# Kernel optimization log

Hardware: AMD Instinct MI355X
Metric: run time of the kernel (lower is better)

Reference implementation:

```python
import jax, jax.numpy as jnp
import numpy as np

N = 50000
EPS = 1e-4
NUM_CLASSES = 10
PROTOS_PER_CLASS = 5


def setup_inputs() -> dict:
    key = jax.random.key(0)
    ks = jax.random.split(key, 12)
    x = jax.random.normal(ks[0], (N, 512), dtype=jnp.float32)
    edge_index = jax.random.randint(ks[1], (2, 640000), 0, N, dtype=jnp.int64)
    # GCNConv weights (PyG: y = x @ W^T + b after aggregation)
    def glorot(k, o, i):
        s = jnp.sqrt(6.0 / (o + i)).astype(jnp.float32)
        return jax.random.uniform(k, (o, i), jnp.float32, -s, s)
    W1 = glorot(ks[2], 128, 512); b1 = jnp.zeros((128,), jnp.float32)
    W2 = glorot(ks[3], 128, 128); b2 = jnp.zeros((128,), jnp.float32)
    W3 = glorot(ks[4], 128, 128); b3 = jnp.zeros((128,), jnp.float32)
    prototype_vectors = jax.random.uniform(ks[5], (NUM_CLASSES * PROTOS_PER_CLASS, 128), jnp.float32)
    # last layer: +1 for prototype's own class, -0.5 elsewhere, no bias
    proto_class = jnp.arange(NUM_CLASSES * PROTOS_PER_CLASS) // PROTOS_PER_CLASS  # [P]
    identity = (proto_class[None, :] == jnp.arange(NUM_CLASSES)[:, None]).astype(jnp.float32)  # [C,P]
    last_w = 1.0 * identity + (-0.5) * (1.0 - identity)
    return {"x": x, "edge_index": edge_index, "W1": W1, "b1": b1, "W2": W2,
            "b2": b2, "W3": W3, "b3": b3,
            "prototype_vectors": prototype_vectors, "last_w": last_w}


def _gcn_conv(h, src, dst, deg_inv_sqrt, W, b):
    # h: [N,Fin]; messages from src -> dst with symmetric norm; self-loops included in src/dst
    m = h @ W.T                                   # [N,Fout]
    norm = deg_inv_sqrt[src] * deg_inv_sqrt[dst]  # [E+N]
    out = jax.ops.segment_sum(norm[:, None] * m[src], dst, num_segments=N)
    return out + b


def reference(x, edge_index, W1, b1, W2, b2, W3, b3, prototype_vectors, last_w):
    # add self loops once; degree computed on targets (PyG gcn_norm)
    loop = jnp.arange(N, dtype=edge_index.dtype)
    src = jnp.concatenate([edge_index[0], loop])
    dst = jnp.concatenate([edge_index[1], loop])
    deg = jax.ops.segment_sum(jnp.ones_like(src, dtype=x.dtype), dst, num_segments=N)
    deg_inv_sqrt = jnp.where(deg > 0, jax.lax.rsqrt(deg), 0.0)

    h = jax.nn.relu(_gcn_conv(x, src, dst, deg_inv_sqrt, W1, b1))
    h = jax.nn.relu(_gcn_conv(h, src, dst, deg_inv_sqrt, W2, b2))
    h = jax.nn.relu(_gcn_conv(h, src, dst, deg_inv_sqrt, W3, b3))
    emb = h  # [N,128]

    xp = emb @ prototype_vectors.T                                    # [N,P]
    distance = (-2.0 * xp + jnp.sum(emb * emb, axis=1, keepdims=True)
                + jnp.sum(prototype_vectors * prototype_vectors, axis=1)[None, :])
    similarity = jnp.log((distance + 1.0) / (distance + EPS))         # [N,P]
    logits = similarity @ last_w.T                                    # [N,C]
    probs = jax.nn.softmax(logits, axis=-1)
    return logits, probs, emb, distance
```

## Files before the change

### kernel.cpp

```cpp
#include <hip/hip_runtime.h>
#include <cstdint>
#include <cstddef>

#define NFEAT 128
#define NPROTO 50
#define NCLS 10

typedef __attribute__((ext_vector_type(8))) short short8;
typedef __attribute__((ext_vector_type(4))) float floatx4;
typedef _Float16 halfv8 __attribute__((ext_vector_type(8)));


__global__ __launch_bounds__(256) void count_kernel(const int* __restrict__ dst,
                                                    int* __restrict__ cnt, int E) {
  int e = blockIdx.x * 256 + threadIdx.x;
  if (e < E) atomicAdd(&cnt[dst[e]], 1);
}


__global__ __launch_bounds__(256)
void scan1_kernel(const int* __restrict__ cnt, int* __restrict__ row_ptr,
                  int* __restrict__ btot, int Nn) {
  __shared__ int s[256];
  int t = threadIdx.x;
  int i = blockIdx.x * 256 + t;
  int v = (i < Nn) ? cnt[i] : 0;
  s[t] = v;
  __syncthreads();
#pragma unroll
  for (int off = 1; off < 256; off <<= 1) {
    int add = (t >= off) ? s[t - off] : 0;
    __syncthreads();
    s[t] += add;
    __syncthreads();
  }
  if (i < Nn) row_ptr[i] = s[t] - v;
  if (t == 255) btot[blockIdx.x] = s[255];
}

__global__ __launch_bounds__(256)
void scan2_kernel(const int* __restrict__ btot, int* __restrict__ boff,
                  int* __restrict__ row_ptr, int nb, int Nn) {
  __shared__ int s[256];
  int t = threadIdx.x;
  int v = (t < nb) ? btot[t] : 0;
  s[t] = v;
  __syncthreads();
#pragma unroll
  for (int off = 1; off < 256; off <<= 1) {
    int add = (t >= off) ? s[t - off] : 0;
    __syncthreads();
    s[t] += add;
    __syncthreads();
  }
  if (t < nb) boff[t] = s[t] - v;
  if (t == 255) row_ptr[Nn] = s[255];
}

__global__ __launch_bounds__(256)
void scan3_kernel(int* __restrict__ row_ptr, const int* __restrict__ boff,
                  const int* __restrict__ cnt, float* __restrict__ dis, int Nn) {
  int i = blockIdx.x * 256 + threadIdx.x;
  if (i < Nn) {
    row_ptr[i] += boff[blockIdx.x];
    dis[i] = 1.0f / sqrtf((float)(cnt[i] + 1));
  }
}

__global__ __launch_bounds__(256) void fill_kernel(const int* __restrict__ src,
                                                   const int* __restrict__ dst,
                                                   const int* __restrict__ row_ptr,
                                                   int* __restrict__ cursor,
                                                   int* __restrict__ csr_src, int E) {
  int e = blockIdx.x * 256 + threadIdx.x;
  if (e < E) {
    int d = dst[e];
    int pos = atomicAdd(&cursor[d], 1);
    csr_src[row_ptr[d] + pos] = src[e];
  }
}


__device__ __forceinline__ void split1(float v, unsigned short& h, unsigned short& l) {
  unsigned int b = __float_as_uint(v);
  h = (unsigned short)(b >> 16);
  float r = v - __uint_as_float(b & 0xFFFF0000u);
  l = (unsigned short)(__float_as_uint(r) >> 16);
}

__global__ __launch_bounds__(256) void wconv_kernel(const float* __restrict__ W,
                                                    unsigned short* __restrict__ Wh,
                                                    unsigned short* __restrict__ Wl, int n) {
  int i = blockIdx.x * 256 + threadIdx.x;
  if (i < n) {
    unsigned short h, l;
    split1(W[i], h, l);
    Wh[i] = h; Wl[i] = l;
  }
}

__global__ __launch_bounds__(128)
void psplit_kernel(const float* __restrict__ proto, unsigned short* __restrict__ Ph,
                   unsigned short* __restrict__ Pl, float* __restrict__ pn) {
  int t = threadIdx.x;
  for (int idx = t; idx < 64 * 128; idx += 128) {
    int p = idx >> 7;
    float v = (p < NPROTO) ? proto[p * 128 + (idx & 127)] : 0.f;
    unsigned short h, l;
    split1(v, h, l);
    Ph[idx] = h; Pl[idx] = l;
  }
  if (t < 64) {
    float s = 0.f;
    if (t < NPROTO)
      for (int f = 0; f < 128; ++f) { float v = proto[t * 128 + f]; s += v * v; }
    pn[t] = s;
  }
}


__global__ __launch_bounds__(512, 2)
void gemm_p1(const float* __restrict__ A, const float* __restrict__ dis,
             const unsigned short* __restrict__ Wh, const unsigned short* __restrict__ Wl,
             _Float16* __restrict__ C, int M) {
  __shared__ short8 Wlds[4096];
  int t = threadIdx.x;
  int w = t >> 6, lane = t & 63;
  int col = lane & 15, quad = lane >> 4;
  int ntiles = (M + 15) >> 4;
  int tile = blockIdx.x * 8 + w;
  if (tile >= ntiles) tile = ntiles - 1;
  int m0 = tile * 16;

  floatx4 acc[8];
#pragma unroll
  for (int b = 0; b < 8; ++b) acc[b] = floatx4{0.f, 0.f, 0.f, 0.f};

  int r = m0 + col;
  int row = r < M ? r : M - 1;
  float dsc = dis[row];

  for (int p = 0; p < 4; ++p) {
    const int kb = p * 128;
    __syncthreads();
#pragma unroll
    for (int i = 0; i < 8; ++i) {
      int u = i * 512 + t;
      int pl_ = u >> 11;
      int v = u & 2047;
      int g = v >> 8, q = (v >> 4) & 15, c = v & 15;
      const unsigned short* srcp = (pl_ ? Wl : Wh) + (size_t)(g * 16 + c) * 512 + kb + q * 8;
      __builtin_amdgcn_global_load_lds(
          (const __attribute__((address_space(1))) void*)srcp,
          (__attribute__((address_space(3))) void*)((char*)Wlds + (size_t)(i * 512 + w * 64) * 16),
          16, 0, 0);
    }
    float4 pf[4][2];
#pragma unroll
    for (int c0 = 0; c0 < 4; ++c0) {
      const float* pp = A + (size_t)row * 512 + kb + c0 * 32 + quad * 8;
      pf[c0][0] = *(const float4*)pp;
      pf[c0][1] = *(const float4*)(pp + 4);
    }
    __syncthreads();

#pragma unroll
    for (int ck = 0; ck < 4; ++ck) {
      float4 va = pf[ck][0];
      float4 vb = pf[ck][1];
      float f[8] = {va.x, va.y, va.z, va.w, vb.x, vb.y, vb.z, vb.w};
      short8 ah, al;
#pragma unroll
      for (int j = 0; j < 8; ++j) {
        unsigned short h, l;
        split1(f[j] * dsc, h, l);
        ah[j] = (short)h; al[j] = (short)l;
      }
#pragma unroll
      for (int nt = 0; nt < 8; ++nt) {
        int u = nt * 256 + (ck * 4 + quad) * 16 + col;
        short8 bh = Wlds[u];
        short8 bl = Wlds[2048 + u];
        acc[nt] = __builtin_amdgcn_mfma_f32_16x16x32_bf16(ah, bh, acc[nt], 0, 0, 0);
        acc[nt] = __builtin_amdgcn_mfma_f32_16x16x32_bf16(al, bh, acc[nt], 0, 0, 0);
        acc[nt] = __builtin_amdgcn_mfma_f32_16x16x32_bf16(ah, bl, acc[nt], 0, 0, 0);
      }
    }
  }

#pragma unroll
  for (int rr = 0; rr < 4; ++rr) {
    int m = m0 + quad * 4 + rr;
    if (m < M) {
#pragma unroll
      for (int nt = 0; nt < 8; ++nt)
        C[(size_t)m * NFEAT + nt * 16 + col] = (_Float16)acc[nt][rr];
    }
  }
}


__global__ __launch_bounds__(512, 2)
void gemm_p2(const unsigned short* __restrict__ Ah, const unsigned short* __restrict__ Al,
             const unsigned short* __restrict__ Wh, const unsigned short* __restrict__ Wl,
             _Float16* __restrict__ C, int M) {
  __shared__ short8 Wlds[4096];
  int t = threadIdx.x;
  int w = t >> 6, lane = t & 63;
  int col = lane & 15, quad = lane >> 4;
  int ntiles = (M + 31) >> 5;
  int tile = blockIdx.x * 8 + w;
  if (tile >= ntiles) tile = ntiles - 1;
  int m0 = tile * 32;

  floatx4 acc[2][8];
#pragma unroll
  for (int a = 0; a < 2; ++a)
#pragma unroll
    for (int b = 0; b < 8; ++b) acc[a][b] = floatx4{0.f, 0.f, 0.f, 0.f};

  int row[2];
#pragma unroll
  for (int mt = 0; mt < 2; ++mt) {
    int r = m0 + mt * 16 + col;
    row[mt] = r < M ? r : M - 1;
  }

#pragma unroll
  for (int i = 0; i < 4; ++i) {
    int u = i * 512 + t;
    int g = u >> 8, q = (u >> 4) & 15, c = u & 15;
    size_t off = (size_t)(g * 16 + c) * 128 + q * 8;
    char* dst = (char*)Wlds + (size_t)(i * 512 + w * 64) * 16;
    __builtin_amdgcn_global_load_lds(
        (const __attribute__((address_space(1))) void*)(Wh + off),
        (__attribute__((address_space(3))) void*)dst, 16, 0, 0);
    __builtin_amdgcn_global_load_lds(
        (const __attribute__((address_space(1))) void*)(Wl + off),
        (__attribute__((address_space(3))) void*)(dst + 32768), 16, 0, 0);
  }

  short8 pah[4][2], pal[4][2];
#pragma unroll
  for (int ck = 0; ck < 4; ++ck)
#pragma unroll
    for (int mt = 0; mt < 2; ++mt) {
      size_t off = (size_t)row[mt] * 128 + ck * 32 + quad * 8;
      pah[ck][mt] = *(const short8*)(Ah + off);
      pal[ck][mt] = *(const short8*)(Al + off);
    }

  __syncthreads();

#pragma unroll
  for (int ck = 0; ck < 4; ++ck) {
#pragma unroll
    for (int nt = 0; nt < 8; ++nt) {
      int u = (nt * 16 + ck * 4 + quad) * 16 + col;
      short8 bh = Wlds[u];
      short8 bl = Wlds[2048 + u];
#pragma unroll
      for (int mt = 0; mt < 2; ++mt) {
        acc[mt][nt] = __builtin_amdgcn_mfma_f32_16x16x32_bf16(pah[ck][mt], bh, acc[mt][nt], 0, 0, 0);
        acc[mt][nt] = __builtin_amdgcn_mfma_f32_16x16x32_bf16(pal[ck][mt], bh, acc[mt][nt], 0, 0, 0);
        acc[mt][nt] = __builtin_amdgcn_mfma_f32_16x16x32_bf16(pah[ck][mt], bl, acc[mt][nt], 0, 0, 0);
      }
    }
  }

#pragma unroll
  for (int mt = 0; mt < 2; ++mt)
#pragma unroll
    for (int r = 0; r < 4; ++r) {
      int m = m0 + mt * 16 + quad * 4 + r;
      if (m < M) {
#pragma unroll
        for (int nt = 0; nt < 8; ++nt)
          C[(size_t)m * NFEAT + nt * 16 + col] = (_Float16)acc[mt][nt][r];
      }
    }
}


template<int MODE>
__global__ __launch_bounds__(256)
void agg_kernel(const _Float16* __restrict__ m, const int* __restrict__ row_ptr,
                const int* __restrict__ csr_src, const float* __restrict__ dis,
                const float* __restrict__ bias,
                unsigned int* __restrict__ out_h, unsigned int* __restrict__ out_l,
                float* __restrict__ out_f, int Nn) {
  int t = threadIdx.x;
  int w = t >> 6, lane = t & 63;
  int sub = lane >> 4, l = lane & 15;
  int i = blockIdx.x * 16 + w * 4 + sub;
  if (i >= Nn) return;
  const halfv8* m8 = (const halfv8*)m;
  halfv8 sv = m8[(size_t)i * 16 + l];
  float acc[8];
#pragma unroll
  for (int j = 0; j < 8; ++j) acc[j] = (float)sv[j];
  int e0 = row_ptr[i], e1 = row_ptr[i + 1];
  int e = e0;
  for (; e + 4 <= e1; e += 4) {
    int s0 = csr_src[e], s1 = csr_src[e + 1], s2 = csr_src[e + 2], s3 = csr_src[e + 3];
    halfv8 v0 = m8[(size_t)s0 * 16 + l];
    halfv8 v1 = m8[(size_t)s1 * 16 + l];
    halfv8 v2 = m8[(size_t)s2 * 16 + l];
    halfv8 v3 = m8[(size_t)s3 * 16 + l];
#pragma unroll
    for (int j = 0; j < 8; ++j)
      acc[j] += ((float)v0[j] + (float)v1[j]) + ((float)v2[j] + (float)v3[j]);
  }
  for (; e < e1; ++e) {
    int s = csr_src[e];
    halfv8 v = m8[(size_t)s * 16 + l];
#pragma unroll
    for (int j = 0; j < 8; ++j) acc[j] += (float)v[j];
  }
  float di = dis[i];
  float4 ba = ((const float4*)bias)[l * 2];
  float4 bb = ((const float4*)bias)[l * 2 + 1];
  float bv[8] = {ba.x, ba.y, ba.z, ba.w, bb.x, bb.y, bb.z, bb.w};
  float r[8];
#pragma unroll
  for (int j = 0; j < 8; ++j) r[j] = fmaxf(fmaf(di, acc[j], bv[j]), 0.f);
  if (MODE == 0) {
    unsigned int ph[4], pl[4];
#pragma unroll
    for (int j = 0; j < 4; ++j) {
      unsigned short h0, l0, h1, l1;
      split1(di * r[2 * j], h0, l0);
      split1(di * r[2 * j + 1], h1, l1);
      ph[j] = (unsigned int)h0 | ((unsigned int)h1 << 16);
      pl[j] = (unsigned int)l0 | ((unsigned int)l1 << 16);
    }
    ((uint4*)out_h)[(size_t)i * 16 + l] = make_uint4(ph[0], ph[1], ph[2], ph[3]);
    ((uint4*)out_l)[(size_t)i * 16 + l] = make_uint4(pl[0], pl[1], pl[2], pl[3]);
  } else {
    ((float4*)out_f)[(size_t)i * 32 + l * 2] = make_float4(r[0], r[1], r[2], r[3]);
    ((float4*)out_f)[(size_t)i * 32 + l * 2 + 1] = make_float4(r[4], r[5], r[6], r[7]);
  }
}


__global__ __launch_bounds__(256)
void proto_mfma(const float* __restrict__ emb,
                const unsigned short* __restrict__ Ph, const unsigned short* __restrict__ Pl,
                const float* __restrict__ pn, const float* __restrict__ lastw,
                float* __restrict__ out_logits, float* __restrict__ out_probs,
                float* __restrict__ out_dist, int Nn) {
  __shared__ float simS[64][65];
  int t = threadIdx.x;
  int w = t >> 6, lane = t & 63;
  int col = lane & 15, quad = lane >> 4;
  int m0 = blockIdx.x * 64 + w * 16;
  int row = m0 + col;
  int r0 = row < Nn ? row : Nn - 1;

  floatx4 acc[4];
#pragma unroll
  for (int nt = 0; nt < 4; ++nt) acc[nt] = floatx4{0.f, 0.f, 0.f, 0.f};

  float en = 0.f;
  const float* ap = emb + (size_t)r0 * 128 + quad * 8;
#pragma unroll
  for (int kc = 0; kc < 4; ++kc) {
    float4 va = *(const float4*)(ap + kc * 32);
    float4 vb = *(const float4*)(ap + kc * 32 + 4);
    float f[8] = {va.x, va.y, va.z, va.w, vb.x, vb.y, vb.z, vb.w};
    short8 ah, al;
#pragma unroll
    for (int j = 0; j < 8; ++j) {
      unsigned short h, l;
      split1(f[j], h, l);
      ah[j] = (short)h; al[j] = (short)l;
      en = fmaf(f[j], f[j], en);
    }
#pragma unroll
    for (int nt = 0; nt < 4; ++nt) {
      const unsigned short* bp = Ph + (size_t)(nt * 16 + col) * 128 + kc * 32 + quad * 8;
      const unsigned short* bq = Pl + (size_t)(nt * 16 + col) * 128 + kc * 32 + quad * 8;
      short8 bh = *(const short8*)bp;
      short8 bl = *(const short8*)bq;
      acc[nt] = __builtin_amdgcn_mfma_f32_16x16x32_bf16(ah, bh, acc[nt], 0, 0, 0);
      acc[nt] = __builtin_amdgcn_mfma_f32_16x16x32_bf16(al, bh, acc[nt], 0, 0, 0);
      acc[nt] = __builtin_amdgcn_mfma_f32_16x16x32_bf16(ah, bl, acc[nt], 0, 0, 0);
    }
  }
  en += __shfl_xor(en, 16);
  en += __shfl_xor(en, 32);

  float pnv[4];
#pragma unroll
  for (int nt = 0; nt < 4; ++nt) pnv[nt] = pn[nt * 16 + col];

#pragma unroll
  for (int r = 0; r < 4; ++r) {
    int node = m0 + quad * 4 + r;
    float enr = __shfl(en, quad * 4 + r);
    bool valid = node < Nn;
#pragma unroll
    for (int nt = 0; nt < 4; ++nt) {
      int p = nt * 16 + col;
      float d = enr - 2.f * acc[nt][r] + pnv[nt];
      float sim = (p < NPROTO) ? logf((d + 1.0f) / (d + 1e-4f)) : 0.f;
      simS[w * 16 + quad * 4 + r][p] = sim;
      if (valid && p < NPROTO) out_dist[(size_t)node * NPROTO + p] = d;
    }
  }
  __syncthreads();

  if (t < 64) {
    int node = blockIdx.x * 64 + t;
    if (node < Nn) {
      float sims[NPROTO];
#pragma unroll
      for (int p = 0; p < NPROTO; ++p) sims[p] = simS[t][p];
      float lg[NCLS];
      float mx = -1e30f;
#pragma unroll
      for (int c = 0; c < NCLS; ++c) {
        float s = 0.f;
#pragma unroll
        for (int p = 0; p < NPROTO; ++p) s = fmaf(sims[p], lastw[c * NPROTO + p], s);
        lg[c] = s;
        mx = fmaxf(mx, s);
      }
      float ss = 0.f;
#pragma unroll
      for (int c = 0; c < NCLS; ++c) ss += expf(lg[c] - mx);
      float inv = 1.f / ss;
#pragma unroll
      for (int c = 0; c < NCLS; ++c) {
        out_logits[(size_t)node * NCLS + c] = lg[c];
        out_probs[(size_t)node * NCLS + c] = expf(lg[c] - mx) * inv;
      }
    }
  }
}


extern "C" void kernel_launch(void* const* d_in, const int* in_sizes, int n_in,
                              void* d_out, int out_size, void* d_ws, size_t ws_size,
                              hipStream_t stream) {
  const float* x    = (const float*)d_in[0];
  const int*  eidx  = (const int*)d_in[1];
  const float* W1   = (const float*)d_in[2];
  const float* b1   = (const float*)d_in[3];
  const float* W2   = (const float*)d_in[4];
  const float* b2   = (const float*)d_in[5];
  const float* W3   = (const float*)d_in[6];
  const float* b3   = (const float*)d_in[7];
  const float* prot = (const float*)d_in[8];
  const float* lastw= (const float*)d_in[9];

  const int Nn = in_sizes[0] / 512;
  const int E  = in_sizes[1] / 2;
  const int* esrc = eidx;
  const int* edst = eidx + E;

  float* out        = (float*)d_out;
  float* out_logits = out;
  float* out_probs  = out + (size_t)Nn * NCLS;
  float* out_emb    = out + (size_t)Nn * 2 * NCLS;
  float* out_dist   = out_emb + (size_t)Nn * NFEAT;

  _Float16* mbuf = (_Float16*)d_ws;
  unsigned int* hh = (unsigned int*)(mbuf + (size_t)Nn * NFEAT);
  unsigned int* hl = hh + (size_t)Nn * 64;
  unsigned short* W1h = (unsigned short*)(hl + (size_t)Nn * 64);
  unsigned short* W1l = W1h + 128 * 512;
  unsigned short* W2h = W1l + 128 * 512;
  unsigned short* W2l = W2h + 128 * 128;
  unsigned short* W3h = W2l + 128 * 128;
  unsigned short* W3l = W3h + 128 * 128;
  unsigned short* Ph  = W3l + 128 * 128;
  unsigned short* Pl  = Ph + 64 * 128;
  float* pn    = (float*)(Pl + 64 * 128);
  int* cnt     = (int*)(pn + 64);
  float* dis   = (float*)(cnt + Nn);
  int* row_ptr = (int*)(dis + Nn);
  int* cursor  = row_ptr + Nn + 1;
  int* btot    = cursor + Nn;
  int* boff    = btot + 256;
  int* csr_src = boff + 256;

  const int nb = (Nn + 255) / 256;

  hipMemsetAsync(cnt, 0, Nn * sizeof(int), stream);
  hipMemsetAsync(cursor, 0, Nn * sizeof(int), stream);
  count_kernel<<<(E + 255) / 256, 256, 0, stream>>>(edst, cnt, E);
  scan1_kernel<<<nb, 256, 0, stream>>>(cnt, row_ptr, btot, Nn);
  scan2_kernel<<<1, 256, 0, stream>>>(btot, boff, row_ptr, nb, Nn);
  scan3_kernel<<<nb, 256, 0, stream>>>(row_ptr, boff, cnt, dis, Nn);
  fill_kernel<<<(E + 255) / 256, 256, 0, stream>>>(esrc, edst, row_ptr, cursor, csr_src, E);

  wconv_kernel<<<(128 * 512 + 255) / 256, 256, 0, stream>>>(W1, W1h, W1l, 128 * 512);
  wconv_kernel<<<(128 * 128 + 255) / 256, 256, 0, stream>>>(W2, W2h, W2l, 128 * 128);
  wconv_kernel<<<(128 * 128 + 255) / 256, 256, 0, stream>>>(W3, W3h, W3l, 128 * 128);
  psplit_kernel<<<1, 128, 0, stream>>>(prot, Ph, Pl, pn);

  int ntiles16 = (Nn + 15) / 16;
  int p1blocks = (ntiles16 + 7) / 8;
  int ntiles32 = (Nn + 31) / 32;
  int gblocks = (ntiles32 + 7) / 8;
  int ablocks = (Nn + 15) / 16;
  gemm_p1<<<p1blocks, 512, 0, stream>>>(x, dis, W1h, W1l, mbuf, Nn);
  agg_kernel<0><<<ablocks, 256, 0, stream>>>(mbuf, row_ptr, csr_src, dis, b1, hh, hl, nullptr, Nn);
  gemm_p2<<<gblocks, 512, 0, stream>>>((const unsigned short*)hh, (const unsigned short*)hl,
                                       W2h, W2l, mbuf, Nn);
  agg_kernel<0><<<ablocks, 256, 0, stream>>>(mbuf, row_ptr, csr_src, dis, b2, hh, hl, nullptr, Nn);
  gemm_p2<<<gblocks, 512, 0, stream>>>((const unsigned short*)hh, (const unsigned short*)hl,
                                       W3h, W3l, mbuf, Nn);
  agg_kernel<1><<<ablocks, 256, 0, stream>>>(mbuf, row_ptr, csr_src, dis, b3, nullptr, nullptr, out_emb, Nn);

  proto_mfma<<<(Nn + 63) / 64, 256, 0, stream>>>(out_emb, Ph, Pl, pn, lastw,
                                                 out_logits, out_probs, out_dist, Nn);
}
```

Baseline: 434.6 us.

## Merge preprocessing launches and replace three-pass scan with decoupled single-pass scan

Folds the weight/prototype bf16 splitting, prototype norms and the zeroing of the count/cursor/state buffers into one grid-stride prep kernel, replacing two memsets and four small launches. Replaces the three-kernel prefix scan with a single-pass scan where each block publishes its tile sum through flagged atomics and sums all predecessors' totals. The aim is to cut launch count and inter-kernel gaps in the graph-building phase. The single-pass scan relies on earlier blocks being scheduled, which holds for about 196 blocks, and each block does O(b) spin loads.

```diff
diff --git a/kernel.cpp b/kernel.cpp
--- a/kernel.cpp
+++ b/kernel.cpp
@@ -9,6 +9,48 @@
 typedef __attribute__((ext_vector_type(8))) short short8;
 typedef __attribute__((ext_vector_type(4))) float floatx4;
 typedef _Float16 halfv8 __attribute__((ext_vector_type(8)));
+
+
+__device__ __forceinline__ void split1(float v, unsigned short& h, unsigned short& l) {
+  unsigned int b = __float_as_uint(v);
+  h = (unsigned short)(b >> 16);
+  float r = v - __uint_as_float(b & 0xFFFF0000u);
+  l = (unsigned short)(__float_as_uint(r) >> 16);
+}
+
+
+__global__ __launch_bounds__(256)
+void prep_kernel(const float* __restrict__ W1, const float* __restrict__ W2,
+                 const float* __restrict__ W3, const float* __restrict__ proto,
+                 unsigned short* __restrict__ W1h, unsigned short* __restrict__ W1l,
+                 unsigned short* __restrict__ W2h, unsigned short* __restrict__ W2l,
+                 unsigned short* __restrict__ W3h, unsigned short* __restrict__ W3l,
+                 unsigned short* __restrict__ Ph, unsigned short* __restrict__ Pl,
+                 float* __restrict__ pn, int* __restrict__ zero_base, int zero_n) {
+  int g = blockIdx.x * 256 + threadIdx.x;
+  int stride = gridDim.x * 256;
+  for (int i = g; i < 128 * 512; i += stride) {
+    unsigned short h, l; split1(W1[i], h, l); W1h[i] = h; W1l[i] = l;
+  }
+  for (int i = g; i < 128 * 128; i += stride) {
+    unsigned short h, l; split1(W2[i], h, l); W2h[i] = h; W2l[i] = l;
+  }
+  for (int i = g; i < 128 * 128; i += stride) {
+    unsigned short h, l; split1(W3[i], h, l); W3h[i] = h; W3l[i] = l;
+  }
+  for (int i = g; i < 64 * 128; i += stride) {
+    int p = i >> 7;
+    float v = (p < NPROTO) ? proto[p * 128 + (i & 127)] : 0.f;
+    unsigned short h, l; split1(v, h, l); Ph[i] = h; Pl[i] = l;
+  }
+  for (int i = g; i < zero_n; i += stride) zero_base[i] = 0;
+  if (g < 64) {
+    float s = 0.f;
+    if (g < NPROTO)
+      for (int f = 0; f < 128; ++f) { float v = proto[g * 128 + f]; s += v * v; }
+    pn[g] = s;
+  }
+}
 
 
 __global__ __launch_bounds__(256) void count_kernel(const int* __restrict__ dst,
@@ -19,11 +61,14 @@
 
 
 __global__ __launch_bounds__(256)
-void scan1_kernel(const int* __restrict__ cnt, int* __restrict__ row_ptr,
-                  int* __restrict__ btot, int Nn) {
+void scan_lb_kernel(const int* __restrict__ cnt, int* __restrict__ row_ptr,
+                    float* __restrict__ dis,
+                    unsigned long long* __restrict__ state, int Nn) {
   __shared__ int s[256];
+  __shared__ int exc_s;
+  int b = blockIdx.x;
   int t = threadIdx.x;
-  int i = blockIdx.x * 256 + t;
+  int i = b * 256 + t;
   int v = (i < Nn) ? cnt[i] : 0;
   s[t] = v;
   __syncthreads();
@@ -34,37 +79,32 @@
     s[t] += add;
     __syncthreads();
   }
-  if (i < Nn) row_ptr[i] = s[t] - v;
-  if (t == 255) btot[blockIdx.x] = s[255];
-}
-
-__global__ __launch_bounds__(256)
-void scan2_kernel(const int* __restrict__ btot, int* __restrict__ boff,
-                  int* __restrict__ row_ptr, int nb, int Nn) {
-  __shared__ int s[256];
-  int t = threadIdx.x;
-  int v = (t < nb) ? btot[t] : 0;
-  s[t] = v;
+  int tile_sum = s[255];
+  if (t == 0) {
+    unsigned long long pkt = (1ULL << 32) | (unsigned int)tile_sum;
+    __hip_atomic_store(&state[b], pkt, __ATOMIC_RELEASE, __HIP_MEMORY_SCOPE_AGENT);
+    if (b == 0) exc_s = 0;
+  }
+  if (b > 0 && t < 64) {
+    int acc = 0;
+    for (int p = t; p < b; p += 64) {
+      unsigned long long pk;
+      do {
+        pk = __hip_atomic_load(&state[p], __ATOMIC_ACQUIRE, __HIP_MEMORY_SCOPE_AGENT);
+      } while ((pk >> 32) == 0);
+      acc += (int)(unsigned int)pk;
+    }
+#pragma unroll
+    for (int off = 32; off; off >>= 1) acc += __shfl_down(acc, off);
+    if (t == 0) exc_s = acc;
+  }
   __syncthreads();
-#pragma unroll
-  for (int off = 1; off < 256; off <<= 1) {
-    int add = (t >= off) ? s[t - off] : 0;
-    __syncthreads();
-    s[t] += add;
-    __syncthreads();
-  }
-  if (t < nb) boff[t] = s[t] - v;
-  if (t == 255) row_ptr[Nn] = s[255];
-}
-
-__global__ __launch_bounds__(256)
-void scan3_kernel(int* __restrict__ row_ptr, const int* __restrict__ boff,
-                  const int* __restrict__ cnt, float* __restrict__ dis, int Nn) {
-  int i = blockIdx.x * 256 + threadIdx.x;
+  int exc = exc_s;
   if (i < Nn) {
-    row_ptr[i] += boff[blockIdx.x];
-    dis[i] = 1.0f / sqrtf((float)(cnt[i] + 1));
-  }
+    row_ptr[i] = exc + s[t] - v;
+    dis[i] = 1.0f / sqrtf((float)(v + 1));
+  }
+  if (b == gridDim.x - 1 && t == 0) row_ptr[Nn] = exc + tile_sum;
 }
 
 __global__ __launch_bounds__(256) void fill_kernel(const int* __restrict__ src,
@@ -77,44 +117,6 @@
     int d = dst[e];
     int pos = atomicAdd(&cursor[d], 1);
     csr_src[row_ptr[d] + pos] = src[e];
-  }
-}
-
-
-__device__ __forceinline__ void split1(float v, unsigned short& h, unsigned short& l) {
-  unsigned int b = __float_as_uint(v);
-  h = (unsigned short)(b >> 16);
-  float r = v - __uint_as_float(b & 0xFFFF0000u);
-  l = (unsigned short)(__float_as_uint(r) >> 16);
-}
-
-__global__ __launch_bounds__(256) void wconv_kernel(const float* __restrict__ W,
-                                                    unsigned short* __restrict__ Wh,
-                                                    unsigned short* __restrict__ Wl, int n) {
-  int i = blockIdx.x * 256 + threadIdx.x;
-  if (i < n) {
-    unsigned short h, l;
-    split1(W[i], h, l);
-    Wh[i] = h; Wl[i] = l;
-  }
-}
-
-__global__ __launch_bounds__(128)
-void psplit_kernel(const float* __restrict__ proto, unsigned short* __restrict__ Ph,
-                   unsigned short* __restrict__ Pl, float* __restrict__ pn) {
-  int t = threadIdx.x;
-  for (int idx = t; idx < 64 * 128; idx += 128) {
-    int p = idx >> 7;
-    float v = (p < NPROTO) ? proto[p * 128 + (idx & 127)] : 0.f;
-    unsigned short h, l;
-    split1(v, h, l);
-    Ph[idx] = h; Pl[idx] = l;
-  }
-  if (t < 64) {
-    float s = 0.f;
-    if (t < NPROTO)
-      for (int f = 0; f < 128; ++f) { float v = proto[t * 128 + f]; s += v * v; }
-    pn[t] = s;
   }
 }
 
@@ -477,28 +479,21 @@
   unsigned short* Ph  = W3l + 128 * 128;
   unsigned short* Pl  = Ph + 64 * 128;
   float* pn    = (float*)(Pl + 64 * 128);
-  int* cnt     = (int*)(pn + 64);
-  float* dis   = (float*)(cnt + Nn);
+  unsigned long long* state = (unsigned long long*)(pn + 64);
+  int* cnt     = (int*)(state + 256);
+  int* cursor  = cnt + Nn;
+  float* dis   = (float*)(cursor + Nn);
   int* row_ptr = (int*)(dis + Nn);
-  int* cursor  = row_ptr + Nn + 1;
-  int* btot    = cursor + Nn;
-  int* boff    = btot + 256;
-  int* csr_src = boff + 256;
+  int* csr_src = row_ptr + Nn + 1;
 
   const int nb = (Nn + 255) / 256;
-
-  hipMemsetAsync(cnt, 0, Nn * sizeof(int), stream);
-  hipMemsetAsync(cursor, 0, Nn * sizeof(int), stream);
+  const int zero_n = 512 + 2 * Nn;
+
+  prep_kernel<<<128, 256, 0, stream>>>(W1, W2, W3, prot, W1h, W1l, W2h, W2l,
+                                       W3h, W3l, Ph, Pl, pn, (int*)state, zero_n);
   count_kernel<<<(E + 255) / 256, 256, 0, stream>>>(edst, cnt, E);
-  scan1_kernel<<<nb, 256, 0, stream>>>(cnt, row_ptr, btot, Nn);
-  scan2_kernel<<<1, 256, 0, stream>>>(btot, boff, row_ptr, nb, Nn);
-  scan3_kernel<<<nb, 256, 0, stream>>>(row_ptr, boff, cnt, dis, Nn);
+  scan_lb_kernel<<<nb, 256, 0, stream>>>(cnt, row_ptr, dis, state, Nn);
   fill_kernel<<<(E + 255) / 256, 256, 0, stream>>>(esrc, edst, row_ptr, cursor, csr_src, E);
-
-  wconv_kernel<<<(128 * 512 + 255) / 256, 256, 0, stream>>>(W1, W1h, W1l, 128 * 512);
-  wconv_kernel<<<(128 * 128 + 255) / 256, 256, 0, stream>>>(W2, W2h, W2l, 128 * 128);
-  wconv_kernel<<<(128 * 128 + 255) / 256, 256, 0, stream>>>(W3, W3h, W3l, 128 * 128);
-  psplit_kernel<<<1, 128, 0, stream>>>(prot, Ph, Pl, pn);
 
   int ntiles16 = (Nn + 15) / 16;
   int p1blocks = (ntiles16 + 7) / 8;
```

Result: faster. 397.8 us (-8.5%).
